# Kernel tuning notes

Hardware: AMD Instinct MI355X
Metric: run time of the kernel (lower is better)

The kernel has to match this reference:

```python
import jax, jax.numpy as jnp
import numpy as np

EPS = 1e-5   # BatchNorm eps
TAU = 0.1    # gumbel-softmax temperature (self.temperature)
N_LOCAL = 32 # max_local_num
B, M, D, S = 4, 8192, 64, 1024
MLP = [32, 128]


def setup_inputs() -> dict:
    key = jax.random.key(0)
    ks = jax.random.split(key, 12)
    coordinate = jax.random.normal(ks[0], (B, M, 3), dtype=jnp.float32)
    feature = jax.random.normal(ks[1], (B, M, D), dtype=jnp.float32)
    u = jax.random.uniform(ks[2], (B, S, M), dtype=jnp.float32, minval=1e-6, maxval=1.0 - 1e-6)
    gumbel_noise = -jnp.log(-jnp.log(u))
    w0 = jax.random.normal(ks[3], (5, MLP[0]), dtype=jnp.float32) * (1.0 / np.sqrt(5))
    w1 = jax.random.normal(ks[4], (MLP[0], MLP[1]), dtype=jnp.float32) * (1.0 / np.sqrt(MLP[0]))
    w2 = jax.random.normal(ks[5], (MLP[1], S), dtype=jnp.float32) * (1.0 / np.sqrt(MLP[1]))
    bn0_gamma = 1.0 + 0.1 * jax.random.normal(ks[6], (MLP[0],), dtype=jnp.float32)
    bn0_beta = 0.1 * jax.random.normal(ks[7], (MLP[0],), dtype=jnp.float32)
    bn0_mean = 0.1 * jax.random.normal(ks[8], (MLP[0],), dtype=jnp.float32)
    bn0_var = jax.random.uniform(ks[9], (MLP[0],), dtype=jnp.float32, minval=0.5, maxval=1.5)
    bn1_gamma = 1.0 + 0.1 * jax.random.normal(ks[10], (MLP[1],), dtype=jnp.float32)
    bn1_beta = 0.1 * jax.random.normal(ks[11], (MLP[1],), dtype=jnp.float32)
    k2 = jax.random.split(jax.random.fold_in(key, 7), 2)
    bn1_mean = 0.1 * jax.random.normal(k2[0], (MLP[1],), dtype=jnp.float32)
    bn1_var = jax.random.uniform(k2[1], (MLP[1],), dtype=jnp.float32, minval=0.5, maxval=1.5)
    return dict(coordinate=coordinate, feature=feature, gumbel_noise=gumbel_noise,
                w0=w0, bn0_gamma=bn0_gamma, bn0_beta=bn0_beta, bn0_mean=bn0_mean, bn0_var=bn0_var,
                w1=w1, bn1_gamma=bn1_gamma, bn1_beta=bn1_beta, bn1_mean=bn1_mean, bn1_var=bn1_var,
                w2=w2)


def _bn(x, gamma, beta, mean, var):
    # BatchNorm1d in inference form over the channel (last) dim
    return (x - mean) * jax.lax.rsqrt(var + EPS) * gamma + beta


def reference(coordinate, feature, gumbel_noise,
              w0, bn0_gamma, bn0_beta, bn0_mean, bn0_var,
              w1, bn1_gamma, bn1_beta, bn1_mean, bn1_var,
              w2):
    # spherical features: [x, y, z, theta, phi] -> [B, m, 5]
    r = jnp.linalg.norm(coordinate, axis=-1)
    th = jnp.arccos(coordinate[..., 2] / r)
    fi = jnp.arctan2(coordinate[..., 1], coordinate[..., 0])
    c2 = jnp.concatenate([coordinate, th[..., None], fi[..., None]], axis=-1)
    # per-point MLP with BN + ReLU
    h = jax.nn.relu(_bn(c2 @ w0, bn0_gamma, bn0_beta, bn0_mean, bn0_var))
    h = jax.nn.relu(_bn(h @ w1, bn1_gamma, bn1_beta, bn1_mean, bn1_var))
    logits = h @ w2                        # [B, m, s]
    Q = jax.nn.sigmoid(jnp.swapaxes(logits, 1, 2))  # [B, s, m]
    # topk grouping over points
    _, idx = jax.lax.top_k(Q, N_LOCAL)     # [B, s, n]
    b_idx = jnp.arange(coordinate.shape[0])[:, None, None]
    grouped_points = coordinate[b_idx, idx]   # [B, s, n, 3]
    grouped_feature = feature[b_idx, idx]     # [B, s, n, d]
    # gumbel-softmax (hard, straight-through) sampling over points
    y_soft = jax.nn.softmax((Q + gumbel_noise) / TAU, axis=-1)
    hard_idx = jnp.argmax(y_soft, axis=-1)
    y_hard = jax.nn.one_hot(hard_idx, Q.shape[-1], dtype=Q.dtype)
    Qg = y_hard - jax.lax.stop_gradient(y_soft) + y_soft  # [B, s, m]
    sampled_points = Qg @ coordinate        # [B, s, 3]
    sampled_feature = Qg @ feature          # [B, s, d]
    grouped_feature = grouped_feature.at[:, :, 0, :].set(sampled_feature)
    return sampled_points, grouped_points, sampled_feature, grouped_feature, Qg
```

## Files before the change

kernel.cpp:

```cpp
#include <hip/hip_runtime.h>
#include <math.h>

#define Bd   4
#define Md   8192
#define Dd   64
#define Sd   1024
#define H0d  32
#define H1d  128

#define OFF_SP 0
#define OFF_GP 12288
#define OFF_SF 405504
#define OFF_GF 667648
#define OFF_QG 9056256

#define CAP 512

__device__ __forceinline__ unsigned f2u(float f) {
    unsigned v = __float_as_uint(f);
    return (v & 0x80000000u) ? ~v : (v | 0x80000000u);
}

__global__ __launch_bounds__(256) void k1_mlp(
    const float* __restrict__ coord,
    const float* __restrict__ w0,
    const float* __restrict__ g0, const float* __restrict__ be0,
    const float* __restrict__ mu0, const float* __restrict__ va0,
    const float* __restrict__ w1,
    const float* __restrict__ g1, const float* __restrict__ be1,
    const float* __restrict__ mu1, const float* __restrict__ va1,
    float* __restrict__ h1T)
{
    const int jg = blockIdx.x & 3;
    const int j0 = jg * 32;
    __shared__ double W1[H0d * 32];
    __shared__ double W0[5 * H0d];
    __shared__ double MU0[H0d], RS0[H0d], BE0[H0d];
    __shared__ double MU1[32], RS1[32], BE1[32];
    const int t = threadIdx.x;
    for (int e = t; e < H0d * 32; e += 256) {
        int i = e >> 5, jc = e & 31;
        W1[e] = (double)w1[i * H1d + j0 + jc];
    }
    if (t < 5 * H0d) W0[t] = (double)w0[t];
    if (t < H0d) {
        MU0[t] = (double)mu0[t];
        RS0[t] = (double)g0[t] / sqrt((double)va0[t] + 1e-5);
        BE0[t] = (double)be0[t];
    }
    if (t >= 192 && t < 224) {
        int j = t - 192;
        MU1[j] = (double)mu1[j0 + j];
        RS1[j] = (double)g1[j0 + j] / sqrt((double)va1[j0 + j] + 1e-5);
        BE1[j] = (double)be1[j0 + j];
    }
    __syncthreads();

    const int p = (blockIdx.x >> 2) * 256 + t;
    const double x = (double)coord[p * 3 + 0];
    const double y = (double)coord[p * 3 + 1];
    const double z = (double)coord[p * 3 + 2];
    const double r  = sqrt(x * x + y * y + z * z);
    const double th = acos(z / r);
    const double fi = atan2(y, x);

    double h0[H0d];
    #pragma unroll
    for (int i = 0; i < H0d; i++) {
        double a = x * W0[i] + y * W0[H0d + i] + z * W0[2 * H0d + i]
                 + th * W0[3 * H0d + i] + fi * W0[4 * H0d + i];
        a = (a - MU0[i]) * RS0[i] + BE0[i];
        h0[i] = a > 0.0 ? a : 0.0;
    }
    float* o = h1T + (size_t)(p >> 13) * (H1d * Md) + (p & (Md - 1));
    for (int jc = 0; jc < 32; jc += 2) {
        double a0 = 0.0, a1 = 0.0;
        #pragma unroll
        for (int i = 0; i < H0d; i++) {
            double h = h0[i];
            a0 += h * W1[i * 32 + jc];
            a1 += h * W1[i * 32 + jc + 1];
        }
        a0 = (a0 - MU1[jc]) * RS1[jc] + BE1[jc];             a0 = a0 > 0.0 ? a0 : 0.0;
        a1 = (a1 - MU1[jc + 1]) * RS1[jc + 1] + BE1[jc + 1]; a1 = a1 > 0.0 ? a1 : 0.0;
        o[(size_t)(j0 + jc) * Md]     = (float)a0;
        o[(size_t)(j0 + jc + 1) * Md] = (float)a1;
    }
}

__global__ __launch_bounds__(256, 4) void k2_gemm(
    const float* __restrict__ h1T,
    const float* __restrict__ w2,
    unsigned* __restrict__ uqout)
{
    __shared__ float As[32][128];
    __shared__ float Bs[32][128];
    const int bx = blockIdx.x, b = blockIdx.y;
    const int mtile = bx & 63, stile = bx >> 6;
    const int m0 = mtile * 128, s0 = stile * 128;
    const int t = threadIdx.x;
    const int tm = t & 15, tn = t >> 4;

    float acc[8][8] = {};

    for (int kt = 0; kt < 4; kt++) {
        const float* Ag = h1T + ((size_t)b * H1d + kt * 32) * Md + m0;
        const float* Bg = w2 + (size_t)(kt * 32) * Sd + s0;
        #pragma unroll
        for (int i = 0; i < 4; i++) {
            int idx = t + i * 256;
            int kk = idx >> 5, c = idx & 31;
            *(float4*)&As[kk][c * 4] = *(const float4*)&Ag[(size_t)kk * Md + c * 4];
            *(float4*)&Bs[kk][c * 4] = *(const float4*)&Bg[(size_t)kk * Sd + c * 4];
        }
        __syncthreads();

        #pragma unroll 8
        for (int k = 0; k < 32; k++) {
            float a_[8], b_[8];
            *(float4*)&a_[0] = *(const float4*)&As[k][tm * 4];
            *(float4*)&a_[4] = *(const float4*)&As[k][64 + tm * 4];
            *(float4*)&b_[0] = *(const float4*)&Bs[k][tn * 4];
            *(float4*)&b_[4] = *(const float4*)&Bs[k][64 + tn * 4];
            #pragma unroll
            for (int si = 0; si < 8; si++)
                #pragma unroll
                for (int mi = 0; mi < 8; mi++)
                    acc[si][mi] += b_[si] * a_[mi];
        }
        __syncthreads();
    }

    #pragma unroll
    for (int si = 0; si < 8; si++) {
        int s = s0 + (si >> 2) * 64 + tn * 4 + (si & 3);
        unsigned* row = uqout + ((size_t)b * Sd + s) * Md + m0;
        uint4 w0v, w1v;
        w0v.x = f2u(1.0f / (1.0f + expf(-acc[si][0])));
        w0v.y = f2u(1.0f / (1.0f + expf(-acc[si][1])));
        w0v.z = f2u(1.0f / (1.0f + expf(-acc[si][2])));
        w0v.w = f2u(1.0f / (1.0f + expf(-acc[si][3])));
        w1v.x = f2u(1.0f / (1.0f + expf(-acc[si][4])));
        w1v.y = f2u(1.0f / (1.0f + expf(-acc[si][5])));
        w1v.z = f2u(1.0f / (1.0f + expf(-acc[si][6])));
        w1v.w = f2u(1.0f / (1.0f + expf(-acc[si][7])));
        *(uint4*)&row[tm * 4]      = w0v;
        *(uint4*)&row[64 + tm * 4] = w1v;
    }
}

__global__ __launch_bounds__(256) void k3_fused(
    unsigned* __restrict__ uqbuf,
    const float* __restrict__ gumbel,
    const float* __restrict__ coord,
    const float* __restrict__ feat,
    float* __restrict__ out)
{
    const int r = blockIdx.x;
    const int b = r >> 10;
    const int t = threadIdx.x;
    const int lane = t & 63, wav = t >> 6;
    const uint4*  L4 = (const uint4*)(uqbuf + (size_t)r * Md);
    const float4* G4 = (const float4*)(gumbel + (size_t)r * Md);

    __shared__ unsigned long long wred[2][4];
    __shared__ unsigned long long ck[CAP];
    __shared__ unsigned swT[4];
    __shared__ int cnt;
    __shared__ int order[32];

    unsigned uq[32];
    unsigned gbu = 0u; int gbm = 0;
    #pragma unroll
    for (int j = 0; j < 8; j++) {
        uint4  v = L4[j * 256 + t];
        float4 g = G4[j * 256 + t];
        #pragma unroll
        for (int c = 0; c < 4; c++) {
            unsigned u = ((const unsigned*)&v)[c];
            uq[j * 4 + c] = u;
            float q = __uint_as_float(u ^ 0x80000000u);
            unsigned us = f2u(q + ((const float*)&g)[c]);
            if (us > gbu) { gbu = us; gbm = j * 1024 + t * 4 + c; }
        }
    }

    {
        unsigned long long key = ((unsigned long long)gbu << 32) | (unsigned)(Md - 1 - gbm);
        #pragma unroll
        for (int o = 32; o > 0; o >>= 1) {
            unsigned long long other = __shfl_down(key, o);
            if (other > key) key = other;
        }
        if (lane == 0) wred[0][wav] = key;
    }
    if (t == 0) cnt = 0;
    __syncthreads();
    unsigned long long gbest = wred[0][0];
    if (wred[0][1] > gbest) gbest = wred[0][1];
    if (wred[0][2] > gbest) gbest = wred[0][2];
    if (wred[0][3] > gbest) gbest = wred[0][3];
    const int am = Md - 1 - (int)(gbest & 0xFFFFFFFFull);

    unsigned pm = 0u;
    #pragma unroll
    for (int i = 0; i < 32; i++) pm = max(pm, uq[i]);
    unsigned v = pm;
    #pragma unroll
    for (int k = 2; k <= 64; k <<= 1) {
        #pragma unroll
        for (int j = k >> 1; j > 0; j >>= 1) {
            unsigned o = __shfl_xor(v, j);
            bool up = ((lane & k) == 0);
            bool lower = ((lane & j) == 0);
            unsigned mn = min(v, o), mx = max(v, o);
            v = (lower == up) ? mn : mx;
        }
    }
    unsigned tw = __shfl(v, 32);
    if (lane == 0) swT[wav] = tw;
    __syncthreads();
    const unsigned T = max(max(swT[0], swT[1]), max(swT[2], swT[3]));

    #pragma unroll
    for (int i = 0; i < 32; i++) {
        if (uq[i] >= T) {
            int pos = atomicAdd(&cnt, 1);
            if (pos < CAP) {
                int m = (i >> 2) * 1024 + t * 4 + (i & 3);
                ck[pos] = ((unsigned long long)uq[i] << 32) | (unsigned)(Md - 1 - m);
            }
        }
    }
    __syncthreads();
    const int n = cnt;

    if (n >= 32 && n <= CAP) {
        for (int j2 = t; j2 < n; j2 += 256) {
            unsigned long long mine = ck[j2];
            int rk = 0;
            for (int i2 = 0; i2 < n; i2++) rk += (ck[i2] > mine) ? 1 : 0;
            if (rk < 32) order[rk] = Md - 1 - (int)(mine & 0xFFFFFFFFull);
        }
    } else {
        for (int round = 0; round < 32; round++) {
            unsigned bu = 0u; int bi = 0;
            #pragma unroll
            for (int i = 0; i < 32; i++)
                if (uq[i] > bu) { bu = uq[i]; bi = i; }
            int bm = (bi >> 2) * 1024 + t * 4 + (bi & 3);
            unsigned long long key =
                ((unsigned long long)bu << 32) | (unsigned)(Md - 1 - bm);
            #pragma unroll
            for (int o = 32; o > 0; o >>= 1) {
                unsigned long long other = __shfl_down(key, o);
                if (other > key) key = other;
            }
            const int p = round & 1;
            if (lane == 0) wred[p][wav] = key;
            __syncthreads();
            unsigned long long best = wred[p][0];
            if (wred[p][1] > best) best = wred[p][1];
            if (wred[p][2] > best) best = wred[p][2];
            if (wred[p][3] > best) best = wred[p][3];
            const int m_win = Md - 1 - (int)(best & 0xFFFFFFFFull);
            if (((m_win >> 2) & 255) == t)
                uq[(m_win >> 10) * 4 + (m_win & 3)] = 0u;
            if (t == 0) order[round] = m_win;
        }
    }
    __syncthreads();

    {
        const int q4 = am >> 2;
        float4* row = (float4*)(uqbuf + (size_t)r * Md);
        #pragma unroll
        for (int i = 0; i < 8; i++) {
            int idx = i * 256 + t;
            float4 vv = make_float4(0.f, 0.f, 0.f, 0.f);
            if (idx == q4) ((float*)&vv)[am & 3] = 1.0f;
            row[idx] = vv;
        }
    }
    if (t < 3)
        out[OFF_SP + (size_t)r * 3 + t] = coord[((size_t)b * Md + am) * 3 + t];
    if (t >= 32 && t < 128) {
        int e = t - 32;
        int nn = e / 3, c = e - nn * 3;
        out[OFF_GP + (size_t)r * 96 + e] = coord[((size_t)b * Md + order[nn]) * 3 + c];
    }
    const float4* F4  = (const float4*)feat;
    float4* SF4 = (float4*)(out + OFF_SF);
    float4* GF4 = (float4*)(out + OFF_GF);
    if (t < 16) {
        float4 fv = F4[((size_t)b * Md + am) * 16 + t];
        SF4[(size_t)r * 16 + t]  = fv;
        GF4[(size_t)r * 512 + t] = fv;
    }
    for (int e4 = 16 + t; e4 < 512; e4 += 256) {
        int nn = e4 >> 4, d4 = e4 & 15;
        GF4[(size_t)r * 512 + e4] = F4[((size_t)b * Md + order[nn]) * 16 + d4];
    }
}

extern "C" void kernel_launch(void* const* d_in, const int* in_sizes, int n_in,
                              void* d_out, int out_size, void* d_ws, size_t ws_size,
                              hipStream_t stream)
{
    (void)in_sizes; (void)n_in; (void)out_size; (void)d_ws; (void)ws_size;
    const float* coord = (const float*)d_in[0];
    const float* feat  = (const float*)d_in[1];
    const float* gum   = (const float*)d_in[2];
    const float* w0    = (const float*)d_in[3];
    const float* g0    = (const float*)d_in[4];
    const float* be0   = (const float*)d_in[5];
    const float* mu0   = (const float*)d_in[6];
    const float* va0   = (const float*)d_in[7];
    const float* w1    = (const float*)d_in[8];
    const float* g1    = (const float*)d_in[9];
    const float* be1   = (const float*)d_in[10];
    const float* mu1   = (const float*)d_in[11];
    const float* va1   = (const float*)d_in[12];
    const float* w2    = (const float*)d_in[13];

    float*    out  = (float*)d_out;
    float*    h1T  = out + OFF_GF;
    unsigned* uqb  = (unsigned*)(out + OFF_QG);

    k1_mlp   <<<dim3(512),     dim3(256), 0, stream>>>(coord, w0, g0, be0, mu0, va0,
                                                       w1, g1, be1, mu1, va1, h1T);
    k2_gemm  <<<dim3(512, 4),  dim3(256), 0, stream>>>(h1T, w2, uqb);
    k3_fused <<<dim3(4096),    dim3(256), 0, stream>>>(uqb, gum, coord, feat, out);
}
```

Before: 229.9 us.

## Fuse gumbel argmax into GEMM epilogue via atomicMax into workspace

The GEMM epilogue now reads the gumbel noise, adds it to the sigmoid scores, reduces a packed (value,index) key across the 16 threads sharing a row, and atomically maxes it into a per-row workspace entry. The fused top-k kernel no longer streams the gumbel tensor; it only reads the precomputed argmax index. The aim is to move the gumbel read next to data already in registers and drop a block reduction from k3. In exchange it adds a memset launch, global 64-bit atomics and an unrolled-1 epilogue loop in k2.

```diff
diff --git a/kernel.cpp b/kernel.cpp
--- a/kernel.cpp
+++ b/kernel.cpp
@@ -91,7 +91,9 @@
 __global__ __launch_bounds__(256, 4) void k2_gemm(
     const float* __restrict__ h1T,
     const float* __restrict__ w2,
-    unsigned* __restrict__ uqout)
+    const float* __restrict__ gum,
+    unsigned* __restrict__ uqout,
+    unsigned long long* __restrict__ ws)
 {
     __shared__ float As[32][128];
     __shared__ float Bs[32][128];
@@ -131,27 +133,57 @@
         __syncthreads();
     }
 
-    #pragma unroll
+    #pragma unroll 1
     for (int si = 0; si < 8; si++) {
-        int s = s0 + (si >> 2) * 64 + tn * 4 + (si & 3);
-        unsigned* row = uqout + ((size_t)b * Sd + s) * Md + m0;
-        uint4 w0v, w1v;
-        w0v.x = f2u(1.0f / (1.0f + expf(-acc[si][0])));
-        w0v.y = f2u(1.0f / (1.0f + expf(-acc[si][1])));
-        w0v.z = f2u(1.0f / (1.0f + expf(-acc[si][2])));
-        w0v.w = f2u(1.0f / (1.0f + expf(-acc[si][3])));
-        w1v.x = f2u(1.0f / (1.0f + expf(-acc[si][4])));
-        w1v.y = f2u(1.0f / (1.0f + expf(-acc[si][5])));
-        w1v.z = f2u(1.0f / (1.0f + expf(-acc[si][6])));
-        w1v.w = f2u(1.0f / (1.0f + expf(-acc[si][7])));
-        *(uint4*)&row[tm * 4]      = w0v;
-        *(uint4*)&row[64 + tm * 4] = w1v;
+        const int s = s0 + (si >> 2) * 64 + tn * 4 + (si & 3);
+        const int row = b * Sd + s;
+        float q0 = 1.0f / (1.0f + expf(-acc[si][0]));
+        float q1 = 1.0f / (1.0f + expf(-acc[si][1]));
+        float q2 = 1.0f / (1.0f + expf(-acc[si][2]));
+        float q3 = 1.0f / (1.0f + expf(-acc[si][3]));
+        float q4 = 1.0f / (1.0f + expf(-acc[si][4]));
+        float q5 = 1.0f / (1.0f + expf(-acc[si][5]));
+        float q6 = 1.0f / (1.0f + expf(-acc[si][6]));
+        float q7 = 1.0f / (1.0f + expf(-acc[si][7]));
+        unsigned* orow = uqout + (size_t)row * Md + m0;
+        uint4 w0v = make_uint4(f2u(q0), f2u(q1), f2u(q2), f2u(q3));
+        uint4 w1v = make_uint4(f2u(q4), f2u(q5), f2u(q6), f2u(q7));
+        *(uint4*)&orow[tm * 4]      = w0v;
+        *(uint4*)&orow[64 + tm * 4] = w1v;
+        const float* gr = gum + (size_t)row * Md + m0;
+        float4 ga = *(const float4*)&gr[tm * 4];
+        float4 gb = *(const float4*)&gr[64 + tm * 4];
+        unsigned long long kmax;
+        {
+            int mb = m0 + tm * 4;
+            unsigned long long k0 = ((unsigned long long)f2u(q0 + ga.x) << 32) | (unsigned)(Md - 1 - (mb + 0));
+            unsigned long long k1 = ((unsigned long long)f2u(q1 + ga.y) << 32) | (unsigned)(Md - 1 - (mb + 1));
+            unsigned long long k2 = ((unsigned long long)f2u(q2 + ga.z) << 32) | (unsigned)(Md - 1 - (mb + 2));
+            unsigned long long k3 = ((unsigned long long)f2u(q3 + ga.w) << 32) | (unsigned)(Md - 1 - (mb + 3));
+            unsigned long long k4 = ((unsigned long long)f2u(q4 + gb.x) << 32) | (unsigned)(Md - 1 - (mb + 64));
+            unsigned long long k5 = ((unsigned long long)f2u(q5 + gb.y) << 32) | (unsigned)(Md - 1 - (mb + 65));
+            unsigned long long k6 = ((unsigned long long)f2u(q6 + gb.z) << 32) | (unsigned)(Md - 1 - (mb + 66));
+            unsigned long long k7 = ((unsigned long long)f2u(q7 + gb.w) << 32) | (unsigned)(Md - 1 - (mb + 67));
+            kmax = k0 > k1 ? k0 : k1;
+            if (k2 > kmax) kmax = k2;
+            if (k3 > kmax) kmax = k3;
+            if (k4 > kmax) kmax = k4;
+            if (k5 > kmax) kmax = k5;
+            if (k6 > kmax) kmax = k6;
+            if (k7 > kmax) kmax = k7;
+        }
+        #pragma unroll
+        for (int o = 1; o < 16; o <<= 1) {
+            unsigned long long other = __shfl_xor(kmax, o);
+            if (other > kmax) kmax = other;
+        }
+        if (tm == 0) atomicMax(&ws[row], kmax);
     }
 }
 
 __global__ __launch_bounds__(256) void k3_fused(
     unsigned* __restrict__ uqbuf,
-    const float* __restrict__ gumbel,
+    const unsigned long long* __restrict__ ws,
     const float* __restrict__ coord,
     const float* __restrict__ feat,
     float* __restrict__ out)
@@ -160,47 +192,28 @@
     const int b = r >> 10;
     const int t = threadIdx.x;
     const int lane = t & 63, wav = t >> 6;
-    const uint4*  L4 = (const uint4*)(uqbuf + (size_t)r * Md);
-    const float4* G4 = (const float4*)(gumbel + (size_t)r * Md);
+    const uint4* L4 = (const uint4*)(uqbuf + (size_t)r * Md);
 
     __shared__ unsigned long long wred[2][4];
     __shared__ unsigned long long ck[CAP];
     __shared__ unsigned swT[4];
     __shared__ int cnt;
     __shared__ int order[32];
+    __shared__ int am_s;
 
     unsigned uq[32];
-    unsigned gbu = 0u; int gbm = 0;
     #pragma unroll
     for (int j = 0; j < 8; j++) {
-        uint4  v = L4[j * 256 + t];
-        float4 g = G4[j * 256 + t];
-        #pragma unroll
-        for (int c = 0; c < 4; c++) {
-            unsigned u = ((const unsigned*)&v)[c];
-            uq[j * 4 + c] = u;
-            float q = __uint_as_float(u ^ 0x80000000u);
-            unsigned us = f2u(q + ((const float*)&g)[c]);
-            if (us > gbu) { gbu = us; gbm = j * 1024 + t * 4 + c; }
-        }
-    }
-
-    {
-        unsigned long long key = ((unsigned long long)gbu << 32) | (unsigned)(Md - 1 - gbm);
-        #pragma unroll
-        for (int o = 32; o > 0; o >>= 1) {
-            unsigned long long other = __shfl_down(key, o);
-            if (other > key) key = other;
-        }
-        if (lane == 0) wred[0][wav] = key;
-    }
-    if (t == 0) cnt = 0;
-    __syncthreads();
-    unsigned long long gbest = wred[0][0];
-    if (wred[0][1] > gbest) gbest = wred[0][1];
-    if (wred[0][2] > gbest) gbest = wred[0][2];
-    if (wred[0][3] > gbest) gbest = wred[0][3];
-    const int am = Md - 1 - (int)(gbest & 0xFFFFFFFFull);
+        uint4 v = L4[j * 256 + t];
+        uq[j * 4 + 0] = v.x;
+        uq[j * 4 + 1] = v.y;
+        uq[j * 4 + 2] = v.z;
+        uq[j * 4 + 3] = v.w;
+    }
+    if (t == 0) {
+        cnt = 0;
+        am_s = Md - 1 - (int)(ws[r] & 0xFFFFFFFFull);
+    }
 
     unsigned pm = 0u;
     #pragma unroll
@@ -220,6 +233,7 @@
     unsigned tw = __shfl(v, 32);
     if (lane == 0) swT[wav] = tw;
     __syncthreads();
+    const int am = am_s;
     const unsigned T = max(max(swT[0], swT[1]), max(swT[2], swT[3]));
 
     #pragma unroll
@@ -307,7 +321,7 @@
                               void* d_out, int out_size, void* d_ws, size_t ws_size,
                               hipStream_t stream)
 {
-    (void)in_sizes; (void)n_in; (void)out_size; (void)d_ws; (void)ws_size;
+    (void)in_sizes; (void)n_in; (void)out_size; (void)ws_size;
     const float* coord = (const float*)d_in[0];
     const float* feat  = (const float*)d_in[1];
     const float* gum   = (const float*)d_in[2];
@@ -326,9 +340,11 @@
     float*    out  = (float*)d_out;
     float*    h1T  = out + OFF_GF;
     unsigned* uqb  = (unsigned*)(out + OFF_QG);
-
+    unsigned long long* ws = (unsigned long long*)d_ws;
+
+    hipMemsetAsync(d_ws, 0, (size_t)(Bd * Sd) * sizeof(unsigned long long), stream);
     k1_mlp   <<<dim3(512),     dim3(256), 0, stream>>>(coord, w0, g0, be0, mu0, va0,
                                                        w1, g1, be1, mu1, va1, h1T);
-    k2_gemm  <<<dim3(512, 4),  dim3(256), 0, stream>>>(h1T, w2, uqb);
-    k3_fused <<<dim3(4096),    dim3(256), 0, stream>>>(uqb, gum, coord, feat, out);
-}
+    k2_gemm  <<<dim3(512, 4),  dim3(256), 0, stream>>>(h1T, w2, gum, uqb, ws);
+    k3_fused <<<dim3(4096),    dim3(256), 0, stream>>>(uqb, ws, coord, feat, out);
+}
```

New measurement: 443.4 us. 92.9% more time.
